# Performance work log

Hardware: AMD Instinct MI355X
Metric: run time of the kernel (lower is better)

Reference implementation:

```python
import jax, jax.numpy as jnp
import numpy as np

N_NODES = 100000
N_EDGES = 1600000
IN_CH = 512
HID = 64
OUT_CH = 1


def setup_inputs() -> dict:
    key = jax.random.key(0)
    k1, k2, k3, k4 = jax.random.split(key, 4)
    x = jax.random.normal(k1, (N_NODES, IN_CH), dtype=jnp.float32)
    edge_index = jax.random.randint(k2, (2, N_EDGES), 0, N_NODES, dtype=jnp.int64)
    # Glorot-ish init for weights
    W1 = jax.random.normal(k3, (IN_CH, HID), dtype=jnp.float32) / np.sqrt(IN_CH)
    b1 = jnp.zeros((HID,), dtype=jnp.float32)
    W2 = jax.random.normal(k4, (HID, OUT_CH), dtype=jnp.float32) / np.sqrt(HID)
    b2 = jnp.zeros((OUT_CH,), dtype=jnp.float32)
    return {"x": x, "edge_index": edge_index, "W1": W1, "b1": b1, "W2": W2, "b2": b2}


def _gcn_conv(h_in, src, dst, norm, W, b, n_nodes):
    # h_in: [N, F_in]; dense transform first (PyG GCNConv order): [N, F_out]
    h = h_in @ W
    # message = norm_e * h[src]; aggregate by dst (scatter-add)
    msg = h[src] * norm[:, None]                      # [E+N, F_out]
    out = jax.ops.segment_sum(msg, dst, num_segments=n_nodes)
    return out + b


def reference(x, edge_index, W1, b1, W2, b2):
    n_nodes = x.shape[0]
    loop = jnp.arange(n_nodes, dtype=edge_index.dtype)
    # add self-loops (A + I)
    src = jnp.concatenate([edge_index[0], loop])
    dst = jnp.concatenate([edge_index[1], loop])
    # symmetric normalization D^{-1/2} (A+I) D^{-1/2}; deg from dst (col)
    ones = jnp.ones_like(dst, dtype=x.dtype)
    deg = jax.ops.segment_sum(ones, dst, num_segments=n_nodes)
    dinv = jnp.where(deg > 0, jax.lax.rsqrt(deg), 0.0)
    norm = dinv[src] * dinv[dst]                      # [E+N]

    h = _gcn_conv(x, src, dst, norm, W1, b1, n_nodes)
    h = jax.nn.relu(h)
    # dropout is identity at inference (F.dropout with training=False)
    h = _gcn_conv(h, src, dst, norm, W2, b2, n_nodes)
    return jax.nn.sigmoid(h)
```

## Files before the change

### kernel.cpp

```cpp
#include <hip/hip_runtime.h>
#include <hip/hip_bf16.h>
#include <math.h>


#define IN_CH 512
#define HID 64

#define BSHIFT 9
#define BNODES 512
#define MAXBKT 256
#define P1_CHUNK 6144

__global__ __launch_bounds__(256) void bin_kernel(
    const int* __restrict__ src, const int* __restrict__ dst, int E,
    int nbkt, int cap, unsigned* __restrict__ bucket_mem, int* __restrict__ gcur)
{
    __shared__ unsigned pairs[P1_CHUNK];
    __shared__ int hist[MAXBKT];
    __shared__ int cur[MAXBKT];
    __shared__ int base[MAXBKT + 1];
    __shared__ int gbase[MAXBKT];

    const int t = threadIdx.x;
    const int e0 = blockIdx.x * P1_CHUNK;
    const int e1 = min(e0 + P1_CHUNK, E);

    for (int i = t; i < nbkt; i += 256) hist[i] = 0;
    __syncthreads();

    for (int i = e0 + t; i < e1; i += 256)
        atomicAdd(&hist[dst[i] >> BSHIFT], 1);
    __syncthreads();

    {
        int v = (t < nbkt) ? hist[t] : 0;
        int own = v;
        __shared__ int sh[256];
        sh[t] = v;
        __syncthreads();
#pragma unroll
        for (int off = 1; off < 256; off <<= 1) {
            int tmp = (t >= off) ? sh[t - off] : 0;
            __syncthreads();
            sh[t] += tmp;
            __syncthreads();
        }
        if (t < nbkt) {
            base[t] = sh[t] - own;
            cur[t]  = sh[t] - own;
            if (t == nbkt - 1) base[nbkt] = sh[t];
        }
    }
    __syncthreads();

    for (int i = e0 + t; i < e1; i += 256) {
        int d = dst[i];
        int b = d >> BSHIFT;
        int pos = atomicAdd(&cur[b], 1);
        pairs[pos] = ((unsigned)src[i] << BSHIFT) | (unsigned)(d & (BNODES - 1));
    }
    __syncthreads();

    if (t < nbkt) {
        int cnt = base[t + 1] - base[t];
        gbase[t] = (cnt > 0) ? atomicAdd(&gcur[t], cnt) : 0;
    }
    __syncthreads();

    const int w = t >> 6, lane = t & 63;
    for (int b = w; b < nbkt; b += 4) {
        int lo = base[b], cnt = base[b + 1] - lo;
        int gb = gbase[b];
        int take = min(cnt, cap - gb);
        unsigned* out = bucket_mem + (size_t)b * cap + gb;
        for (int k = lane; k < take; k += 64) out[k] = pairs[lo + k];
    }
}

__global__ void scanSmall_kernel(const int* __restrict__ gcur, int* __restrict__ bucketoff,
                                 int* __restrict__ rowstart, int nbkt, int N, int E)
{
    __shared__ int sh[MAXBKT];
    const int t = threadIdx.x;
    int v = (t < nbkt) ? gcur[t] : 0;
    sh[t] = v;
    __syncthreads();
#pragma unroll
    for (int off = 1; off < 256; off <<= 1) {
        int tmp = (t >= off) ? sh[t - off] : 0;
        __syncthreads();
        sh[t] += tmp;
        __syncthreads();
    }
    if (t < nbkt) bucketoff[t] = sh[t] - v;
    if (t == 0) { bucketoff[nbkt] = E; rowstart[N] = E; }
}

__global__ __launch_bounds__(512) void hist512_kernel(
    const unsigned* __restrict__ bucket_mem, const int* __restrict__ gcur,
    const int* __restrict__ bucketoff, int cap,
    int* __restrict__ rowstart, float* __restrict__ dinv, int N)
{
    __shared__ int sh[BNODES];
    const int t = threadIdx.x;
    const int b = blockIdx.x;
    const int cnt = gcur[b];
    const unsigned* bm = bucket_mem + (size_t)b * cap;

    sh[t] = 0;
    __syncthreads();
    for (int i = t; i < cnt; i += 512)
        atomicAdd(&sh[bm[i] & (BNODES - 1)], 1);
    __syncthreads();
    const int deg = sh[t];
    __syncthreads();
#pragma unroll
    for (int off = 1; off < BNODES; off <<= 1) {
        int tmp = (t >= off) ? sh[t - off] : 0;
        __syncthreads();
        sh[t] += tmp;
        __syncthreads();
    }
    const int v = b * BNODES + t;
    if (v < N) {
        rowstart[v] = bucketoff[b] + sh[t] - deg;
        dinv[v] = rsqrtf((float)deg + 1.0f);
    }
}

__global__ __launch_bounds__(512) void fill2_kernel(
    const unsigned* __restrict__ bucket_mem, const int* __restrict__ gcur,
    const int* __restrict__ rowstart, int cap,
    int* __restrict__ csr_src, int N)
{
    __shared__ int cur[BNODES];
    const int t = threadIdx.x;
    const int b = blockIdx.x;
    const int cnt = gcur[b];
    const unsigned* bm = bucket_mem + (size_t)b * cap;
    const int v = b * BNODES + t;
    cur[t] = (v < N) ? rowstart[v] : 0;
    __syncthreads();
    for (int i = t; i < cnt; i += 512) {
        unsigned pv = bm[i];
        int slot = atomicAdd(&cur[pv & (BNODES - 1)], 1);
        csr_src[slot] = (int)(pv >> BSHIFT);
    }
}

#define GROWS 64
#define KCHUNK 64
#define XS_LD 68

__global__ __launch_bounds__(256, 4) void gemm1_kernel(
    const float* __restrict__ x, const float* __restrict__ W1,
    float* __restrict__ h, int N)
{
    __shared__ float xs[GROWS * XS_LD];
    __shared__ float Ws[KCHUNK * HID];
    const int tid = threadIdx.x;
    const int fgrp = tid & 7;
    const int rhalf = tid >> 3;
    const int r0 = blockIdx.x * GROWS;

    float acc0[8], acc1[8];
#pragma unroll
    for (int i = 0; i < 8; ++i) { acc0[i] = 0.f; acc1[i] = 0.f; }

    for (int k0 = 0; k0 < IN_CH; k0 += KCHUNK) {
        {
            const float4* wsrc = (const float4*)(W1 + k0 * HID);
            float4* wdst = (float4*)Ws;
#pragma unroll
            for (int i = 0; i < 4; ++i) wdst[tid + i * 256] = wsrc[tid + i * 256];
        }
#pragma unroll
        for (int i = 0; i < 4; ++i) {
            int lin = tid + i * 256;
            int row = lin >> 4;
            int c4  = lin & 15;
            int grow = r0 + row; if (grow >= N) grow = N - 1;
            float4 v = *(const float4*)(x + (size_t)grow * IN_CH + k0 + c4 * 4);
            *(float4*)(xs + row * XS_LD + c4 * 4) = v;
        }
        __syncthreads();

#pragma unroll 8
        for (int kk = 0; kk < KCHUNK; ++kk) {
            float xv0 = xs[rhalf * XS_LD + kk];
            float xv1 = xs[(rhalf + 32) * XS_LD + kk];
            float4 wa = ((const float4*)Ws)[kk * 16 + fgrp * 2];
            float4 wb = ((const float4*)Ws)[kk * 16 + fgrp * 2 + 1];
            acc0[0] = fmaf(xv0, wa.x, acc0[0]);
            acc0[1] = fmaf(xv0, wa.y, acc0[1]);
            acc0[2] = fmaf(xv0, wa.z, acc0[2]);
            acc0[3] = fmaf(xv0, wa.w, acc0[3]);
            acc0[4] = fmaf(xv0, wb.x, acc0[4]);
            acc0[5] = fmaf(xv0, wb.y, acc0[5]);
            acc0[6] = fmaf(xv0, wb.z, acc0[6]);
            acc0[7] = fmaf(xv0, wb.w, acc0[7]);
            acc1[0] = fmaf(xv1, wa.x, acc1[0]);
            acc1[1] = fmaf(xv1, wa.y, acc1[1]);
            acc1[2] = fmaf(xv1, wa.z, acc1[2]);
            acc1[3] = fmaf(xv1, wa.w, acc1[3]);
            acc1[4] = fmaf(xv1, wb.x, acc1[4]);
            acc1[5] = fmaf(xv1, wb.y, acc1[5]);
            acc1[6] = fmaf(xv1, wb.z, acc1[6]);
            acc1[7] = fmaf(xv1, wb.w, acc1[7]);
        }
        __syncthreads();
    }

    int row0 = r0 + rhalf;
    int row1 = row0 + 32;
    if (row0 < N) {
        float4* o = (float4*)(h + (size_t)row0 * HID + fgrp * 8);
        o[0] = make_float4(acc0[0], acc0[1], acc0[2], acc0[3]);
        o[1] = make_float4(acc0[4], acc0[5], acc0[6], acc0[7]);
    }
    if (row1 < N) {
        float4* o = (float4*)(h + (size_t)row1 * HID + fgrp * 8);
        o[0] = make_float4(acc1[0], acc1[1], acc1[2], acc1[3]);
        o[1] = make_float4(acc1[4], acc1[5], acc1[6], acc1[7]);
    }
}

__global__ void gather1_kernel(const int* __restrict__ rowstart, const int* __restrict__ csr_src,
                               const float* __restrict__ dinv, const float* __restrict__ h,
                               const float* __restrict__ b1, const float* __restrict__ W2,
                               float* __restrict__ sv, int N)
{
    const int lane = threadIdx.x & 63;
    const int wid = (blockIdx.x * blockDim.x + threadIdx.x) >> 6;
    if (wid >= N) return;
    const int rs = rowstart[wid];
    const int re = rowstart[wid + 1];
    const float dv = dinv[wid];

    float acc = dv * h[(size_t)wid * HID + lane];

    for (int base = rs; base < re; base += 64) {
        const int n = min(64, re - base);
        int   sj = 0;
        float dj = 0.f;
        if (base + lane < re) {
            sj = csr_src[base + lane];
            dj = dinv[sj];
        }
        for (int j = 0; j < n; ++j) {
            int   s = __shfl(sj, j);
            float w = __shfl(dj, j);
            acc = fmaf(w, h[(size_t)s * HID + lane], acc);
        }
    }

    float t = fmaxf(acc * dv + b1[lane], 0.0f);
    float p = t * W2[lane];
#pragma unroll
    for (int m = 32; m >= 1; m >>= 1) p += __shfl_xor(p, m);
    if (lane == 0) sv[wid] = p;
}

__global__ void gather2_kernel(const int* __restrict__ rowstart, const int* __restrict__ csr_src,
                               const float* __restrict__ dinv, const float* __restrict__ sv,
                               const float* __restrict__ b2, float* __restrict__ out, int N)
{
    const int i = blockIdx.x * blockDim.x + threadIdx.x;
    if (i >= N) return;
    const int rs = rowstart[i];
    const int re = rowstart[i + 1];
    const float dv = dinv[i];
    float acc = dv * sv[i];
    for (int j = rs; j < re; ++j) {
        int s = csr_src[j];
        acc = fmaf(dinv[s], sv[s], acc);
    }
    float z = acc * dv + b2[0];
    out[i] = 1.0f / (1.0f + expf(-z));
}

extern "C" void kernel_launch(void* const* d_in, const int* in_sizes, int n_in,
                              void* d_out, int out_size, void* d_ws, size_t ws_size,
                              hipStream_t stream)
{
    const float* x  = (const float*)d_in[0];
    const int*   ei = (const int*)d_in[1];
    const float* W1 = (const float*)d_in[2];
    const float* b1 = (const float*)d_in[3];
    const float* W2 = (const float*)d_in[4];
    const float* b2 = (const float*)d_in[5];
    float* out = (float*)d_out;

    const int N = in_sizes[0] / IN_CH;
    const int E = in_sizes[1] / 2;
    const int* src = ei;
    const int* dst = ei + E;

    const int nbkt = (N + BNODES - 1) >> BSHIFT;
    if (nbkt > MAXBKT) return;
    const int cap = E / nbkt + E / (nbkt * 4) + 256;

    char* p = (char*)d_ws;
    float* h          = (float*)p;    p += (size_t)N * HID * sizeof(float);
    int*   csr_src    = (int*)p;      p += (size_t)E * sizeof(int);
    unsigned* bmem    = (unsigned*)p; p += (size_t)nbkt * cap * sizeof(unsigned);
    float* dinv       = (float*)p;    p += (size_t)N * sizeof(float);
    float* sv         = (float*)p;    p += (size_t)N * sizeof(float);
    int*   rowstart   = (int*)p;      p += (size_t)(N + 1) * sizeof(int);
    int*   gcur       = (int*)p;      p += (size_t)MAXBKT * sizeof(int);
    int*   bucketoff  = (int*)p;      p += (size_t)(MAXBKT + 1) * sizeof(int);
    if ((size_t)(p - (char*)d_ws) > ws_size) return;

    hipMemsetAsync(gcur, 0, MAXBKT * sizeof(int), stream);

    const int nbin = (E + P1_CHUNK - 1) / P1_CHUNK;
    bin_kernel<<<nbin, 256, 0, stream>>>(src, dst, E, nbkt, cap, bmem, gcur);
    scanSmall_kernel<<<1, 256, 0, stream>>>(gcur, bucketoff, rowstart, nbkt, N, E);
    hist512_kernel<<<nbkt, 512, 0, stream>>>(bmem, gcur, bucketoff, cap, rowstart, dinv, N);
    fill2_kernel<<<nbkt, 512, 0, stream>>>(bmem, gcur, rowstart, cap, csr_src, N);

    gemm1_kernel<<<(N + GROWS - 1) / GROWS, 256, 0, stream>>>(x, W1, h, N);

    gather1_kernel<<<(N * (HID / 4) + 63) / 64, 256, 0, stream>>>(
        rowstart, csr_src, dinv, h, b1, W2, sv, N);

    gather2_kernel<<<(N + 255) / 256, 256, 0, stream>>>(
        rowstart, csr_src, dinv, sv, b2, out, N);
}
```

Measured before the change: 523.6 us.

## Use split-bf16 MFMA for first GEMM, fuse hist/fill, unroll gather

Replaces the FP32 FMA GEMM with an MFMA kernel. Each fp32 operand is split into hi and lo bf16 parts and four 16x16x32 bf16 MFMAs are issued per tile to keep near-fp32 accuracy. W1 is pre-split and transposed by a small kernel, and the x tile is split on the fly from direct global loads without staging in shared memory. The histogram and CSR fill kernels are merged into one launch, and the gather loop is unrolled by four to expose more independent loads. This risks uncoalesced x loads and some precision loss, since the lo*lo term is only approximate.

```diff
diff --git a/kernel.cpp b/kernel.cpp
--- a/kernel.cpp
+++ b/kernel.cpp
@@ -10,6 +10,14 @@
 #define BNODES 512
 #define MAXBKT 256
 #define P1_CHUNK 6144
+
+typedef short s16x8 __attribute__((ext_vector_type(8)));
+typedef float f32x4 __attribute__((ext_vector_type(4)));
+
+__device__ __forceinline__ unsigned short f2bf_rne(float f) {
+    unsigned u = __float_as_uint(f);
+    return (unsigned short)((u + 0x7fffu + ((u >> 16) & 1u)) >> 16);
+}
 
 __global__ __launch_bounds__(256) void bin_kernel(
     const int* __restrict__ src, const int* __restrict__ dst, int E,
@@ -96,50 +104,40 @@
     if (t == 0) { bucketoff[nbkt] = E; rowstart[N] = E; }
 }
 
-__global__ __launch_bounds__(512) void hist512_kernel(
+__global__ __launch_bounds__(512) void histfill_kernel(
     const unsigned* __restrict__ bucket_mem, const int* __restrict__ gcur,
     const int* __restrict__ bucketoff, int cap,
-    int* __restrict__ rowstart, float* __restrict__ dinv, int N)
+    int* __restrict__ rowstart, float* __restrict__ dinv,
+    int* __restrict__ csr_src, int N)
 {
     __shared__ int sh[BNODES];
-    const int t = threadIdx.x;
-    const int b = blockIdx.x;
-    const int cnt = gcur[b];
-    const unsigned* bm = bucket_mem + (size_t)b * cap;
-
-    sh[t] = 0;
-    __syncthreads();
-    for (int i = t; i < cnt; i += 512)
-        atomicAdd(&sh[bm[i] & (BNODES - 1)], 1);
-    __syncthreads();
-    const int deg = sh[t];
-    __syncthreads();
-#pragma unroll
-    for (int off = 1; off < BNODES; off <<= 1) {
-        int tmp = (t >= off) ? sh[t - off] : 0;
-        __syncthreads();
-        sh[t] += tmp;
-        __syncthreads();
-    }
-    const int v = b * BNODES + t;
-    if (v < N) {
-        rowstart[v] = bucketoff[b] + sh[t] - deg;
-        dinv[v] = rsqrtf((float)deg + 1.0f);
-    }
-}
-
-__global__ __launch_bounds__(512) void fill2_kernel(
-    const unsigned* __restrict__ bucket_mem, const int* __restrict__ gcur,
-    const int* __restrict__ rowstart, int cap,
-    int* __restrict__ csr_src, int N)
-{
     __shared__ int cur[BNODES];
     const int t = threadIdx.x;
     const int b = blockIdx.x;
     const int cnt = gcur[b];
     const unsigned* bm = bucket_mem + (size_t)b * cap;
+
+    sh[t] = 0;
+    __syncthreads();
+    for (int i = t; i < cnt; i += 512)
+        atomicAdd(&sh[bm[i] & (BNODES - 1)], 1);
+    __syncthreads();
+    const int deg = sh[t];
+    __syncthreads();
+#pragma unroll
+    for (int off = 1; off < BNODES; off <<= 1) {
+        int tmp = (t >= off) ? sh[t - off] : 0;
+        __syncthreads();
+        sh[t] += tmp;
+        __syncthreads();
+    }
+    const int rs_v = bucketoff[b] + sh[t] - deg;
     const int v = b * BNODES + t;
-    cur[t] = (v < N) ? rowstart[v] : 0;
+    if (v < N) {
+        rowstart[v] = rs_v;
+        dinv[v] = rsqrtf((float)deg + 1.0f);
+    }
+    cur[t] = rs_v;
     __syncthreads();
     for (int i = t; i < cnt; i += 512) {
         unsigned pv = bm[i];
@@ -148,81 +146,95 @@
     }
 }
 
-#define GROWS 64
-#define KCHUNK 64
-#define XS_LD 68
-
-__global__ __launch_bounds__(256, 4) void gemm1_kernel(
-    const float* __restrict__ x, const float* __restrict__ W1,
+__global__ void wsplit_kernel(const float* __restrict__ W1,
+                              unsigned short* __restrict__ Wt_hi,
+                              unsigned short* __restrict__ Wt_lo)
+{
+    int i = blockIdx.x * 256 + threadIdx.x;
+    if (i >= IN_CH * HID) return;
+    int k = i >> 6, c = i & 63;
+    float f = W1[i];
+    unsigned u = __float_as_uint(f);
+    unsigned short hb = (unsigned short)(u >> 16);
+    float r = f - __uint_as_float(u & 0xffff0000u);
+    Wt_hi[c * IN_CH + k] = hb;
+    Wt_lo[c * IN_CH + k] = f2bf_rne(r);
+}
+
+__global__ __launch_bounds__(256) void gemm_mfma_kernel(
+    const float* __restrict__ x,
+    const unsigned short* __restrict__ Wt_hi, const unsigned short* __restrict__ Wt_lo,
     float* __restrict__ h, int N)
 {
-    __shared__ float xs[GROWS * XS_LD];
-    __shared__ float Ws[KCHUNK * HID];
-    const int tid = threadIdx.x;
-    const int fgrp = tid & 7;
-    const int rhalf = tid >> 3;
-    const int r0 = blockIdx.x * GROWS;
-
-    float acc0[8], acc1[8];
-#pragma unroll
-    for (int i = 0; i < 8; ++i) { acc0[i] = 0.f; acc1[i] = 0.f; }
-
-    for (int k0 = 0; k0 < IN_CH; k0 += KCHUNK) {
-        {
-            const float4* wsrc = (const float4*)(W1 + k0 * HID);
-            float4* wdst = (float4*)Ws;
-#pragma unroll
-            for (int i = 0; i < 4; ++i) wdst[tid + i * 256] = wsrc[tid + i * 256];
-        }
-#pragma unroll
-        for (int i = 0; i < 4; ++i) {
-            int lin = tid + i * 256;
-            int row = lin >> 4;
-            int c4  = lin & 15;
-            int grow = r0 + row; if (grow >= N) grow = N - 1;
-            float4 v = *(const float4*)(x + (size_t)grow * IN_CH + k0 + c4 * 4);
-            *(float4*)(xs + row * XS_LD + c4 * 4) = v;
-        }
-        __syncthreads();
-
-#pragma unroll 8
-        for (int kk = 0; kk < KCHUNK; ++kk) {
-            float xv0 = xs[rhalf * XS_LD + kk];
-            float xv1 = xs[(rhalf + 32) * XS_LD + kk];
-            float4 wa = ((const float4*)Ws)[kk * 16 + fgrp * 2];
-            float4 wb = ((const float4*)Ws)[kk * 16 + fgrp * 2 + 1];
-            acc0[0] = fmaf(xv0, wa.x, acc0[0]);
-            acc0[1] = fmaf(xv0, wa.y, acc0[1]);
-            acc0[2] = fmaf(xv0, wa.z, acc0[2]);
-            acc0[3] = fmaf(xv0, wa.w, acc0[3]);
-            acc0[4] = fmaf(xv0, wb.x, acc0[4]);
-            acc0[5] = fmaf(xv0, wb.y, acc0[5]);
-            acc0[6] = fmaf(xv0, wb.z, acc0[6]);
-            acc0[7] = fmaf(xv0, wb.w, acc0[7]);
-            acc1[0] = fmaf(xv1, wa.x, acc1[0]);
-            acc1[1] = fmaf(xv1, wa.y, acc1[1]);
-            acc1[2] = fmaf(xv1, wa.z, acc1[2]);
-            acc1[3] = fmaf(xv1, wa.w, acc1[3]);
-            acc1[4] = fmaf(xv1, wb.x, acc1[4]);
-            acc1[5] = fmaf(xv1, wb.y, acc1[5]);
-            acc1[6] = fmaf(xv1, wb.z, acc1[6]);
-            acc1[7] = fmaf(xv1, wb.w, acc1[7]);
-        }
-        __syncthreads();
-    }
-
-    int row0 = r0 + rhalf;
-    int row1 = row0 + 32;
-    if (row0 < N) {
-        float4* o = (float4*)(h + (size_t)row0 * HID + fgrp * 8);
-        o[0] = make_float4(acc0[0], acc0[1], acc0[2], acc0[3]);
-        o[1] = make_float4(acc0[4], acc0[5], acc0[6], acc0[7]);
-    }
-    if (row1 < N) {
-        float4* o = (float4*)(h + (size_t)row1 * HID + fgrp * 8);
-        o[0] = make_float4(acc1[0], acc1[1], acc1[2], acc1[3]);
-        o[1] = make_float4(acc1[4], acc1[5], acc1[6], acc1[7]);
-    }
+    const int lane = threadIdx.x & 63;
+    const int wv   = threadIdx.x >> 6;
+    const int r_base = (blockIdx.x * 4 + wv) * 32;
+    if (r_base >= N) return;
+
+    const int mrow = lane & 15;
+    const int kgrp = lane >> 4;
+
+    int ra0 = r_base + mrow;        if (ra0 >= N) ra0 = N - 1;
+    int ra1 = r_base + 16 + mrow;   if (ra1 >= N) ra1 = N - 1;
+    const float* a0p = x + (size_t)ra0 * IN_CH + kgrp * 8;
+    const float* a1p = x + (size_t)ra1 * IN_CH + kgrp * 8;
+
+    f32x4 acc[2][4];
+#pragma unroll
+    for (int m = 0; m < 2; ++m)
+#pragma unroll
+        for (int n = 0; n < 4; ++n) acc[m][n] = (f32x4){0.f, 0.f, 0.f, 0.f};
+
+    for (int k0 = 0; k0 < IN_CH; k0 += 32) {
+        float a0[8], a1[8];
+        *(float4*)&a0[0] = *(const float4*)(a0p + k0);
+        *(float4*)&a0[4] = *(const float4*)(a0p + k0 + 4);
+        *(float4*)&a1[0] = *(const float4*)(a1p + k0);
+        *(float4*)&a1[4] = *(const float4*)(a1p + k0 + 4);
+
+        s16x8 bh[4], bl[4];
+#pragma unroll
+        for (int n = 0; n < 4; ++n) {
+            const size_t off = (size_t)(n * 16 + mrow) * IN_CH + k0 + kgrp * 8;
+            bh[n] = *(const s16x8*)(Wt_hi + off);
+            bl[n] = *(const s16x8*)(Wt_lo + off);
+        }
+
+        s16x8 a0h, a0l, a1h, a1l;
+#pragma unroll
+        for (int j = 0; j < 8; ++j) {
+            unsigned u0 = __float_as_uint(a0[j]);
+            a0h[j] = (short)(u0 >> 16);
+            a0l[j] = (short)f2bf_rne(a0[j] - __uint_as_float(u0 & 0xffff0000u));
+            unsigned u1 = __float_as_uint(a1[j]);
+            a1h[j] = (short)(u1 >> 16);
+            a1l[j] = (short)f2bf_rne(a1[j] - __uint_as_float(u1 & 0xffff0000u));
+        }
+
+#pragma unroll
+        for (int n = 0; n < 4; ++n) {
+            acc[0][n] = __builtin_amdgcn_mfma_f32_16x16x32_bf16(a0h, bh[n], acc[0][n], 0, 0, 0);
+            acc[0][n] = __builtin_amdgcn_mfma_f32_16x16x32_bf16(a0h, bl[n], acc[0][n], 0, 0, 0);
+            acc[0][n] = __builtin_amdgcn_mfma_f32_16x16x32_bf16(a0l, bh[n], acc[0][n], 0, 0, 0);
+            acc[0][n] = __builtin_amdgcn_mfma_f32_16x16x32_bf16(a0l, bl[n], acc[0][n], 0, 0, 0);
+            acc[1][n] = __builtin_amdgcn_mfma_f32_16x16x32_bf16(a1h, bh[n], acc[1][n], 0, 0, 0);
+            acc[1][n] = __builtin_amdgcn_mfma_f32_16x16x32_bf16(a1h, bl[n], acc[1][n], 0, 0, 0);
+            acc[1][n] = __builtin_amdgcn_mfma_f32_16x16x32_bf16(a1l, bh[n], acc[1][n], 0, 0, 0);
+            acc[1][n] = __builtin_amdgcn_mfma_f32_16x16x32_bf16(a1l, bl[n], acc[1][n], 0, 0, 0);
+        }
+    }
+
+#pragma unroll
+    for (int m = 0; m < 2; ++m)
+#pragma unroll
+        for (int r = 0; r < 4; ++r) {
+            int row = r_base + m * 16 + kgrp * 4 + r;
+            if (row < N) {
+#pragma unroll
+                for (int n = 0; n < 4; ++n)
+                    h[(size_t)row * HID + n * 16 + mrow] = acc[m][n][r];
+            }
+        }
 }
 
 __global__ void gather1_kernel(const int* __restrict__ rowstart, const int* __restrict__ csr_src,
@@ -247,7 +259,22 @@
             sj = csr_src[base + lane];
             dj = dinv[sj];
         }
-        for (int j = 0; j < n; ++j) {
+        int j = 0;
+        for (; j + 4 <= n; j += 4) {
+            int   s0 = __shfl(sj, j),     s1 = __shfl(sj, j + 1);
+            int   s2 = __shfl(sj, j + 2), s3 = __shfl(sj, j + 3);
+            float w0 = __shfl(dj, j),     w1 = __shfl(dj, j + 1);
+            float w2 = __shfl(dj, j + 2), w3 = __shfl(dj, j + 3);
+            float h0 = h[(size_t)s0 * HID + lane];
+            float h1 = h[(size_t)s1 * HID + lane];
+            float h2 = h[(size_t)s2 * HID + lane];
+            float h3 = h[(size_t)s3 * HID + lane];
+            acc = fmaf(w0, h0, acc);
+            acc = fmaf(w1, h1, acc);
+            acc = fmaf(w2, h2, acc);
+            acc = fmaf(w3, h3, acc);
+        }
+        for (; j < n; ++j) {
             int   s = __shfl(sj, j);
             float w = __shfl(dj, j);
             acc = fmaf(w, h[(size_t)s * HID + lane], acc);
@@ -309,6 +336,8 @@
     int*   rowstart   = (int*)p;      p += (size_t)(N + 1) * sizeof(int);
     int*   gcur       = (int*)p;      p += (size_t)MAXBKT * sizeof(int);
     int*   bucketoff  = (int*)p;      p += (size_t)(MAXBKT + 1) * sizeof(int);
+    unsigned short* Wt_hi = (unsigned short*)p; p += (size_t)IN_CH * HID * sizeof(unsigned short);
+    unsigned short* Wt_lo = (unsigned short*)p; p += (size_t)IN_CH * HID * sizeof(unsigned short);
     if ((size_t)(p - (char*)d_ws) > ws_size) return;
 
     hipMemsetAsync(gcur, 0, MAXBKT * sizeof(int), stream);
@@ -316,10 +345,11 @@
     const int nbin = (E + P1_CHUNK - 1) / P1_CHUNK;
     bin_kernel<<<nbin, 256, 0, stream>>>(src, dst, E, nbkt, cap, bmem, gcur);
     scanSmall_kernel<<<1, 256, 0, stream>>>(gcur, bucketoff, rowstart, nbkt, N, E);
-    hist512_kernel<<<nbkt, 512, 0, stream>>>(bmem, gcur, bucketoff, cap, rowstart, dinv, N);
-    fill2_kernel<<<nbkt, 512, 0, stream>>>(bmem, gcur, rowstart, cap, csr_src, N);
-
-    gemm1_kernel<<<(N + GROWS - 1) / GROWS, 256, 0, stream>>>(x, W1, h, N);
+    histfill_kernel<<<nbkt, 512, 0, stream>>>(bmem, gcur, bucketoff, cap,
+                                              rowstart, dinv, csr_src, N);
+
+    wsplit_kernel<<<(IN_CH * HID + 255) / 256, 256, 0, stream>>>(W1, Wt_hi, Wt_lo);
+    gemm_mfma_kernel<<<(N + 127) / 128, 256, 0, stream>>>(x, Wt_hi, Wt_lo, h, N);
 
     gather1_kernel<<<(N * (HID / 4) + 63) / 64, 256, 0, stream>>>(
         rowstart, csr_src, dinv, h, b1, W2, sv, N);
```

Result: faster. 497.1 us (-5.1%).
